# Optimization experiments

Measured on AMD Instinct MI355X. Metric: run time of the kernel, lower is better.

## Reference

```python
import jax, jax.numpy as jnp
import numpy as np

INPUT_SIZE = 512
HIDDEN_SIZE = 512
FORGET_BIAS = 1.0
B, T = 256, 256


def _xavier_uniform(key, shape):
    fan_out, fan_in = shape
    bound = jnp.sqrt(6.0 / (fan_in + fan_out))
    return jax.random.uniform(key, shape, jnp.float32, -bound, bound)


def setup_inputs() -> dict:
    key = jax.random.key(0)
    k1, k2, k3 = jax.random.split(key, 3)
    H, I = HIDDEN_SIZE, INPUT_SIZE
    x = jax.random.normal(k1, (B, T, I), jnp.float32)
    h0 = jnp.zeros((1, B, H), jnp.float32)
    c0 = jnp.zeros((1, B, H), jnp.float32)
    W_ih = _xavier_uniform(k2, (4 * H, I))
    W_hh = _xavier_uniform(k3, (4 * H, H))
    # biases init to zero, then forget_bias added to [H:2H] of BOTH biases (as in source)
    b = jnp.zeros((4 * H,), jnp.float32).at[H:2 * H].add(FORGET_BIAS)
    return {"input_tensor": x, "h0": h0, "c0": c0,
            "W_ih": W_ih, "W_hh": W_hh, "b_ih": b, "b_hh": b}


def reference(input_tensor, h0, c0, W_ih, W_hh, b_ih, b_hh):
    H = HIDDEN_SIZE
    half = H // 2
    b_all = b_ih + b_hh  # [4H]
    # precompute input projections for all timesteps: [T, B, 4H]
    x_proj = jnp.einsum('bti,gi->tbg', input_tensor, W_ih) + b_all

    def step(carry, xg):
        h, c, m = carry
        gates = xg + h @ W_hh.T                      # [B, 4H]
        i, f, g, o = jnp.split(gates, 4, axis=-1)
        c = jax.nn.sigmoid(f) * c + jax.nn.sigmoid(i) * jnp.tanh(g)
        h = jax.nn.sigmoid(o) * jnp.tanh(c)
        m = jnp.maximum(m, h[:, :half])              # running max over first half
        out = jnp.concatenate([m, h[:, half:]], axis=0)  # torch.cat default dim=0 -> [2B, half]
        return (h, c, m), out

    h_init = h0[0]
    c_init = c0[0]
    m_init = jnp.full((h_init.shape[0], half), -jnp.inf, h_init.dtype)
    (h_n, c_n, _), outs = jax.lax.scan(step, (h_init, c_init, m_init), x_proj)
    all_out = jnp.transpose(outs, (1, 0, 2))         # [2B, T, half]
    return all_out, h_n[None], c_n[None]
```

## Files before the change

### kernel.cpp

```cpp
#include <hip/hip_runtime.h>
#include <cstdint>

#define B_SZ 256
#define T_SZ 256
#define I_SZ 512
#define H_SZ 512
#define HALF 256

typedef __attribute__((ext_vector_type(8))) __bf16 bf16x8;
typedef __attribute__((ext_vector_type(8))) short short8;
typedef __attribute__((ext_vector_type(4))) float f32x4;
typedef __attribute__((ext_vector_type(4))) unsigned int uint4v;

__device__ __forceinline__ unsigned short f2bf(float f) {
  unsigned int u = __float_as_uint(f);
  u = (u + 0x7FFFu + ((u >> 16) & 1u)) >> 16;
  return (unsigned short)u;
}

__device__ __forceinline__ float sigm(float x) {
  return __builtin_amdgcn_rcpf(1.f + __expf(-x));
}
__device__ __forceinline__ float tanh_(float x) {
  float ax = fabsf(x);
  float e = __expf(-2.f * ax);
  float r = (1.f - e) * __builtin_amdgcn_rcpf(1.f + e);
  return copysignf(r, x);
}

__global__ void cvt_f32_bf16(const float* __restrict__ src, unsigned short* __restrict__ dst) {
  long i = ((long)blockIdx.x * 256 + threadIdx.x) * 8;
  float4 a = *(const float4*)(src + i);
  float4 b = *(const float4*)(src + i + 4);
  unsigned int w0 = (unsigned)f2bf(a.x) | ((unsigned)f2bf(a.y) << 16);
  unsigned int w1 = (unsigned)f2bf(a.z) | ((unsigned)f2bf(a.w) << 16);
  unsigned int w2 = (unsigned)f2bf(b.x) | ((unsigned)f2bf(b.y) << 16);
  unsigned int w3 = (unsigned)f2bf(b.z) | ((unsigned)f2bf(b.w) << 16);
  uint4v v = {w0, w1, w2, w3};
  *(uint4v*)(dst + i) = v;
}

__global__ void init_hw(const float* __restrict__ h0, unsigned long long* __restrict__ dst) {
  int i = blockIdx.x * 256 + threadIdx.x;
  unsigned int pw = (unsigned)f2bf(h0[2 * i]) | ((unsigned)f2bf(h0[2 * i + 1]) << 16);
  dst[65536 + i] = (unsigned long long)pw;
  dst[i] = 0xFFFFFFFF00000000ull;
}

__global__ void pack_w(const float* __restrict__ Wih, const float* __restrict__ Whh,
                       unsigned short* __restrict__ wp, unsigned short* __restrict__ hp) {
  int id = blockIdx.x * 256 + threadIdx.x;
  int cid = id & 131071;
  const float* W = (id < 131072) ? Wih : Whh;
  unsigned short* D = (id < 131072) ? wp : hp;
  int l  = cid & 63;
  int ks = (cid >> 6) & 15;
  int nt = (cid >> 10) & 1;
  int w  = (cid >> 11) & 3;
  int hg = (cid >> 13) & 15;
  int row = w * 512 + hg * 32 + nt * 16 + (l & 15);
  int k0  = ks * 32 + (l >> 4) * 8;
  const float* src = W + (long)row * 512 + k0;
  unsigned int wd[4];
#pragma unroll
  for (int j = 0; j < 4; ++j) {
    unsigned int lo = f2bf(src[2 * j]);
    unsigned int hi = f2bf(src[2 * j + 1]);
    wd[j] = lo | (hi << 16);
  }
  uint4v v = {wd[0], wd[1], wd[2], wd[3]};
  *(uint4v*)(D + (long)cid * 8) = v;
}

#define LDPA(dst, base, OFFSTR) \
  asm volatile("global_load_dwordx2 %0, %1, off offset:" OFFSTR " sc0" : "=v"(dst) : "v"(base))
#define LDPS(dst, base, OFFSTR) \
  asm volatile("global_load_dwordx2 %0, %1, off offset:" OFFSTR " sc0 sc1" : "=v"(dst) : "v"(base))
#define LDX16(dst, base, OFFSTR) \
  asm volatile("global_load_dwordx4 %0, %1, off offset:" OFFSTR : "=v"(dst) : "v"(base))

template <int SCOPE>
__device__ __forceinline__ void poll_check(unsigned long long* pv,
                                           const unsigned long long* srcb,
                                           int wv, unsigned tag) {
  bool redo = true;
  while (redo) {
    redo = false;
#pragma unroll
    for (int i = 0; i < 16; ++i) {
      if ((unsigned)(pv[i] >> 32) != tag) {
        const int row = 2 * wv + ((i >> 2) & 1) + (i >> 3) * 8;
        pv[i] = __hip_atomic_load(srcb + row * 256 + (i & 3), __ATOMIC_RELAXED, SCOPE);
        redo = true;
      }
    }
  }
}

template <int SCOPE>
__device__ __forceinline__ void st64(unsigned long long* p, unsigned long long v) {
  __hip_atomic_store(p, v, __ATOMIC_RELAXED, SCOPE);
}

__global__ __launch_bounds__(256, 1) void lstm_main(
    const unsigned short* __restrict__ xb,
    const float* __restrict__ c0,
    const float* __restrict__ b_ih, const float* __restrict__ b_hh,
    const unsigned short* __restrict__ wihp, const unsigned short* __restrict__ whhp,
    unsigned long long* __restrict__ hw64,
    unsigned long long* __restrict__ cnt64,
    float* __restrict__ out)
{
  const int tid  = threadIdx.x;
  const int lane = tid & 63;
  const int w    = tid >> 6;
  const int bg   = blockIdx.x & 15;
  const int hg   = blockIdx.x >> 4;
  const int s0   = hg * 32;
  const int q    = lane >> 4;
  const int c16  = lane & 15;

  __shared__ float glds[4 * 528];
  __shared__ __align__(16) unsigned int hpad[16 * 260];
  __shared__ int s_path;

  int xcd;
  asm volatile("s_getreg_b32 %0, hwreg(20, 0, 32)" : "=s"(xcd));
  xcd &= 15;
  if (tid == 0) {
    unsigned long long inc = 1ull << (8 * xcd);
    __hip_atomic_fetch_add(&cnt64[bg * 8], inc, __ATOMIC_RELAXED, __HIP_MEMORY_SCOPE_SYSTEM);
    unsigned long long m;
    do {
      __builtin_amdgcn_s_sleep(2);
      m = __hip_atomic_load(&cnt64[bg * 8], __ATOMIC_RELAXED, __HIP_MEMORY_SCOPE_SYSTEM);
    } while ((unsigned)((m * 0x0101010101010101ull) >> 56) < 16);
    s_path = (m == (16ull << (8 * xcd))) ? 1 : 0;
  }
  __syncthreads();
  const bool agent_path = (s_path != 0);

  bf16x8 wih[2][16], whh[2][16];
#pragma unroll
  for (int nt = 0; nt < 2; ++nt) {
#pragma unroll
    for (int ks = 0; ks < 16; ++ks) {
      int idc = ((hg * 4 + w) * 2 + nt) * 16 + ks;
      long off = ((long)(idc * 64 + lane)) * 8;
      wih[nt][ks] = __builtin_bit_cast(bf16x8, *(const short8*)(wihp + off));
      whh[nt][ks] = __builtin_bit_cast(bf16x8, *(const short8*)(whhp + off));
    }
  }

  const int jj  = tid & 31;
  const int bl0 = tid >> 5;
  const int bglob0 = bg * 16 + bl0;
  const int bglob1 = bglob0 + 8;
  float bias_v[4];
#pragma unroll
  for (int g = 0; g < 4; ++g)
    bias_v[g] = b_ih[g * 512 + s0 + jj] + b_hh[g * 512 + s0 + jj];
  float cst0 = c0[(long)bglob0 * H_SZ + s0 + jj];
  float cst1 = c0[(long)bglob1 * H_SZ + s0 + jj];
  float m0 = -INFINITY, m1 = -INFINITY;

  const unsigned short* xbase = xb + (long)(bg * 16 + c16) * T_SZ * I_SZ + q * 8;

  const int p   = tid >> 4;
  const int wv  = (tid >> 2) & 3;
  const int cq  = tid & 3;
  const int colbase = p * 16 + cq * 4;

  const int swz = (c16 & 7) << 2;

  bf16x8 xr[16];
  {
    const unsigned short* xn = xbase;
    LDX16(xr[0],  xn, "0");   LDX16(xr[1],  xn, "64");
    LDX16(xr[2],  xn, "128"); LDX16(xr[3],  xn, "192");
    LDX16(xr[4],  xn, "256"); LDX16(xr[5],  xn, "320");
    LDX16(xr[6],  xn, "384"); LDX16(xr[7],  xn, "448");
    LDX16(xr[8],  xn, "512"); LDX16(xr[9],  xn, "576");
    LDX16(xr[10], xn, "640"); LDX16(xr[11], xn, "704");
    LDX16(xr[12], xn, "768"); LDX16(xr[13], xn, "832");
    LDX16(xr[14], xn, "896"); LDX16(xr[15], xn, "960");
  }

#pragma unroll 1
  for (int t = 0; t < T_SZ; ++t) {
    asm volatile("s_waitcnt vmcnt(0)" ::: "memory");
    __builtin_amdgcn_sched_barrier(0);

    const unsigned long long* srcb = hw64 + ((t + 1) & 1) * 65536 + bg * 4096 + colbase;
    const unsigned long long* blo = srcb + 2 * wv * 256;
    const unsigned long long* bhi = blo + 8 * 256;
    unsigned long long pv[16];
    if (agent_path) {
      LDPA(pv[0],  blo, "0");    LDPA(pv[1],  blo, "8");
      LDPA(pv[2],  blo, "16");   LDPA(pv[3],  blo, "24");
      LDPA(pv[4],  blo, "2048"); LDPA(pv[5],  blo, "2056");
      LDPA(pv[6],  blo, "2064"); LDPA(pv[7],  blo, "2072");
      LDPA(pv[8],  bhi, "0");    LDPA(pv[9],  bhi, "8");
      LDPA(pv[10], bhi, "16");   LDPA(pv[11], bhi, "24");
      LDPA(pv[12], bhi, "2048"); LDPA(pv[13], bhi, "2056");
      LDPA(pv[14], bhi, "2064"); LDPA(pv[15], bhi, "2072");
    } else {
      LDPS(pv[0],  blo, "0");    LDPS(pv[1],  blo, "8");
      LDPS(pv[2],  blo, "16");   LDPS(pv[3],  blo, "24");
      LDPS(pv[4],  blo, "2048"); LDPS(pv[5],  blo, "2056");
      LDPS(pv[6],  blo, "2064"); LDPS(pv[7],  blo, "2072");
      LDPS(pv[8],  bhi, "0");    LDPS(pv[9],  bhi, "8");
      LDPS(pv[10], bhi, "16");   LDPS(pv[11], bhi, "24");
      LDPS(pv[12], bhi, "2048"); LDPS(pv[13], bhi, "2056");
      LDPS(pv[14], bhi, "2064"); LDPS(pv[15], bhi, "2072");
    }

    f32x4 acc0 = {0.f, 0.f, 0.f, 0.f};
    f32x4 acc1 = {0.f, 0.f, 0.f, 0.f};
#pragma unroll
    for (int ks = 0; ks < 16; ++ks) {
      bf16x8 a = xr[ks];
      acc0 = __builtin_amdgcn_mfma_f32_16x16x32_bf16(a, wih[0][ks], acc0, 0, 0, 0);
      acc1 = __builtin_amdgcn_mfma_f32_16x16x32_bf16(a, wih[1][ks], acc1, 0, 0, 0);
    }

    asm volatile("s_waitcnt vmcnt(0)" ::: "memory");
    __builtin_amdgcn_sched_barrier(0);

    if (agent_path) poll_check<__HIP_MEMORY_SCOPE_AGENT>(pv, srcb, wv, (unsigned)t);
    else            poll_check<__HIP_MEMORY_SCOPE_SYSTEM>(pv, srcb, wv, (unsigned)t);
#pragma unroll
    for (int g = 0; g < 4; ++g) {
      const int row = 2 * wv + (g & 1) + (g >> 1) * 8;
      const int pc  = colbase ^ ((row & 7) << 2);
      uint4v d = {(unsigned int)pv[g * 4 + 0], (unsigned int)pv[g * 4 + 1],
                  (unsigned int)pv[g * 4 + 2], (unsigned int)pv[g * 4 + 3]};
      *(uint4v*)(hpad + row * 260 + pc) = d;
    }
    __syncthreads();

    {
      const unsigned short* xn = xbase + (long)(t + 1 < T_SZ ? t + 1 : t) * I_SZ;
      LDX16(xr[0],  xn, "0");   LDX16(xr[1],  xn, "64");
      LDX16(xr[2],  xn, "128"); LDX16(xr[3],  xn, "192");
      LDX16(xr[4],  xn, "256"); LDX16(xr[5],  xn, "320");
      LDX16(xr[6],  xn, "384"); LDX16(xr[7],  xn, "448");
      LDX16(xr[8],  xn, "512"); LDX16(xr[9],  xn, "576");
      LDX16(xr[10], xn, "640"); LDX16(xr[11], xn, "704");
      LDX16(xr[12], xn, "768"); LDX16(xr[13], xn, "832");
      LDX16(xr[14], xn, "896"); LDX16(xr[15], xn, "960");
    }

    const unsigned int* hrow = hpad + c16 * 260;
#pragma unroll
    for (int ks = 0; ks < 16; ++ks) {
      bf16x8 a = __builtin_bit_cast(bf16x8,
                   *(const short8*)(hrow + ((ks * 16 + q * 4) ^ swz)));
      acc0 = __builtin_amdgcn_mfma_f32_16x16x32_bf16(a, whh[0][ks], acc0, 0, 0, 0);
      acc1 = __builtin_amdgcn_mfma_f32_16x16x32_bf16(a, whh[1][ks], acc1, 0, 0, 0);
    }

#pragma unroll
    for (int r = 0; r < 4; ++r) {
      glds[w * 528 + (q * 4 + r) * 33 + c16]      = acc0[r];
      glds[w * 528 + (q * 4 + r) * 33 + 16 + c16] = acc1[r];
    }
    __syncthreads();

    float hv0, hv1;
#pragma unroll
    for (int it = 0; it < 2; ++it) {
      int b = bl0 + it * 8;
      float gi = glds[0 * 528 + b * 33 + jj] + bias_v[0];
      float gf = glds[1 * 528 + b * 33 + jj] + bias_v[1];
      float gg = glds[2 * 528 + b * 33 + jj] + bias_v[2];
      float go = glds[3 * 528 + b * 33 + jj] + bias_v[3];
      float& cs = it ? cst1 : cst0;
      cs = sigm(gf) * cs + sigm(gi) * tanh_(gg);
      float h = sigm(go) * tanh_(cs);
      if (it) hv1 = h; else hv0 = h;
    }
    {
      float po0 = __shfl_xor(hv0, 1);
      float po1 = __shfl_xor(hv1, 1);
      if (!(jj & 1)) {
        unsigned long long tagw = (unsigned long long)(t + 1) << 32;
        unsigned long long w0 = tagw | ((unsigned)f2bf(hv0) | ((unsigned)f2bf(po0) << 16));
        unsigned long long w1 = tagw | ((unsigned)f2bf(hv1) | ((unsigned)f2bf(po1) << 16));
        unsigned long long* d0 = hw64 + (t & 1) * 65536 + bg * 4096
                               + bl0 * 256 + (s0 >> 1) + (jj >> 1);
        if (agent_path) {
          st64<__HIP_MEMORY_SCOPE_AGENT>(d0, w0);
          st64<__HIP_MEMORY_SCOPE_AGENT>(d0 + 8 * 256, w1);
        } else {
          st64<__HIP_MEMORY_SCOPE_SYSTEM>(d0, w0);
          st64<__HIP_MEMORY_SCOPE_SYSTEM>(d0 + 8 * 256, w1);
        }
      }
    }

#pragma unroll
    for (int it = 0; it < 2; ++it) {
      int b   = bl0 + it * 8;
      int bgl = bg * 16 + b;
      float h = it ? hv1 : hv0;
      float& mm = it ? m1 : m0;
      if (hg < 8) {
        mm = fmaxf(mm, h);
        out[(long)bgl * (T_SZ * HALF) + t * HALF + s0 + jj] = mm;
      } else {
        out[(long)(256 + bgl) * (T_SZ * HALF) + t * HALF + (s0 - 256) + jj] = h;
      }
      if (t == T_SZ - 1) {
        float cs = it ? cst1 : cst0;
        out[33554432L + (long)bgl * H_SZ + s0 + jj] = h;
        out[33554432L + 131072L + (long)bgl * H_SZ + s0 + jj] = cs;
      }
    }
  }
}

extern "C" void kernel_launch(void* const* d_in, const int* in_sizes, int n_in,
                              void* d_out, int out_size, void* d_ws, size_t ws_size,
                              hipStream_t stream) {
  const float* x   = (const float*)d_in[0];
  const float* h0  = (const float*)d_in[1];
  const float* c0  = (const float*)d_in[2];
  const float* Wih = (const float*)d_in[3];
  const float* Whh = (const float*)d_in[4];
  const float* bih = (const float*)d_in[5];
  const float* bhh = (const float*)d_in[6];
  float* out = (float*)d_out;

  char* ws = (char*)d_ws;
  unsigned short* xb     = (unsigned short*)(ws);
  unsigned short* wihp   = (unsigned short*)(ws + 67108864);
  unsigned short* whhp   = (unsigned short*)(ws + 69206016);
  unsigned long long* hw = (unsigned long long*)(ws + 71303168);
  unsigned long long* cn = (unsigned long long*)(ws + 72351744);

  hipMemsetAsync(cn, 0, 4096, stream);
  cvt_f32_bf16<<<16384, 256, 0, stream>>>(x, xb);
  init_hw<<<256, 256, 0, stream>>>(h0, hw);
  pack_w<<<1024, 256, 0, stream>>>(Wih, Whh, wihp, whhp);
  lstm_main<<<256, 256, 0, stream>>>(xb, c0, bih, bhh, wihp, whhp, hw, cn, out);
}
```

Before: 1.401 ms.

## Streamline per-step recurrence: fast poll check, split accumulators, lighter barriers

Restructures the per-timestep loop of the persistent LSTM kernel. The wait on the x prefetch is relaxed to vmcnt(3), and the tag check now runs a single fast test before falling back to the polling loop. Each MFMA chain is split into two independent accumulators to shorten dependency chains. __syncthreads is replaced by an explicit lgkmcnt wait plus s_barrier, the LDS XOR swizzle is removed, and the h-store work is split so odd and even lanes each issue one store. The risks are LDS bank conflicts from dropping the swizzle and a possibly wrong partial vmcnt wait.

```diff
diff --git a/kernel.cpp b/kernel.cpp
--- a/kernel.cpp
+++ b/kernel.cpp
@@ -80,9 +80,9 @@
   asm volatile("global_load_dwordx4 %0, %1, off offset:" OFFSTR : "=v"(dst) : "v"(base))
 
 template <int SCOPE>
-__device__ __forceinline__ void poll_check(unsigned long long* pv,
-                                           const unsigned long long* srcb,
-                                           int wv, unsigned tag) {
+__device__ __forceinline__ void poll_slow(unsigned long long* pv,
+                                          const unsigned long long* srcb,
+                                          int wv, unsigned tag) {
   bool redo = true;
   while (redo) {
     redo = false;
@@ -171,8 +171,6 @@
   const int cq  = tid & 3;
   const int colbase = p * 16 + cq * 4;
 
-  const int swz = (c16 & 7) << 2;
-
   bf16x8 xr[16];
   {
     const unsigned short* xn = xbase;
@@ -185,10 +183,12 @@
     LDX16(xr[12], xn, "768"); LDX16(xr[13], xn, "832");
     LDX16(xr[14], xn, "896"); LDX16(xr[15], xn, "960");
   }
+  asm volatile("s_waitcnt vmcnt(0)" ::: "memory");
+  __builtin_amdgcn_sched_barrier(0);
 
 #pragma unroll 1
   for (int t = 0; t < T_SZ; ++t) {
-    asm volatile("s_waitcnt vmcnt(0)" ::: "memory");
+    asm volatile("s_waitcnt vmcnt(3)" ::: "memory");
     __builtin_amdgcn_sched_barrier(0);
 
     const unsigned long long* srcb = hw64 + ((t + 1) & 1) * 65536 + bg * 4096 + colbase;
@@ -215,29 +215,42 @@
       LDPS(pv[14], bhi, "2064"); LDPS(pv[15], bhi, "2072");
     }
 
-    f32x4 acc0 = {0.f, 0.f, 0.f, 0.f};
-    f32x4 acc1 = {0.f, 0.f, 0.f, 0.f};
-#pragma unroll
-    for (int ks = 0; ks < 16; ++ks) {
-      bf16x8 a = xr[ks];
-      acc0 = __builtin_amdgcn_mfma_f32_16x16x32_bf16(a, wih[0][ks], acc0, 0, 0, 0);
-      acc1 = __builtin_amdgcn_mfma_f32_16x16x32_bf16(a, wih[1][ks], acc1, 0, 0, 0);
+    f32x4 a0a = {0.f, 0.f, 0.f, 0.f};
+    f32x4 a0b = {0.f, 0.f, 0.f, 0.f};
+    f32x4 a1a = {0.f, 0.f, 0.f, 0.f};
+    f32x4 a1b = {0.f, 0.f, 0.f, 0.f};
+#pragma unroll
+    for (int ks = 0; ks < 16; ks += 2) {
+      a0a = __builtin_amdgcn_mfma_f32_16x16x32_bf16(xr[ks],     wih[0][ks],     a0a, 0, 0, 0);
+      a1a = __builtin_amdgcn_mfma_f32_16x16x32_bf16(xr[ks],     wih[1][ks],     a1a, 0, 0, 0);
+      a0b = __builtin_amdgcn_mfma_f32_16x16x32_bf16(xr[ks + 1], wih[0][ks + 1], a0b, 0, 0, 0);
+      a1b = __builtin_amdgcn_mfma_f32_16x16x32_bf16(xr[ks + 1], wih[1][ks + 1], a1b, 0, 0, 0);
     }
 
     asm volatile("s_waitcnt vmcnt(0)" ::: "memory");
     __builtin_amdgcn_sched_barrier(0);
 
-    if (agent_path) poll_check<__HIP_MEMORY_SCOPE_AGENT>(pv, srcb, wv, (unsigned)t);
-    else            poll_check<__HIP_MEMORY_SCOPE_SYSTEM>(pv, srcb, wv, (unsigned)t);
+    {
+      unsigned ok = 1u;
+#pragma unroll
+      for (int i = 0; i < 16; ++i) ok &= ((unsigned)(pv[i] >> 32) == (unsigned)t) ? 1u : 0u;
+      if (__builtin_expect(ok == 0u, 0)) {
+        if (agent_path) poll_slow<__HIP_MEMORY_SCOPE_AGENT>(pv, srcb, wv, (unsigned)t);
+        else            poll_slow<__HIP_MEMORY_SCOPE_SYSTEM>(pv, srcb, wv, (unsigned)t);
+      }
+    }
+
 #pragma unroll
     for (int g = 0; g < 4; ++g) {
       const int row = 2 * wv + (g & 1) + (g >> 1) * 8;
-      const int pc  = colbase ^ ((row & 7) << 2);
       uint4v d = {(unsigned int)pv[g * 4 + 0], (unsigned int)pv[g * 4 + 1],
                   (unsigned int)pv[g * 4 + 2], (unsigned int)pv[g * 4 + 3]};
-      *(uint4v*)(hpad + row * 260 + pc) = d;
-    }
-    __syncthreads();
+      *(uint4v*)(hpad + row * 260 + colbase) = d;
+    }
+    asm volatile("s_waitcnt lgkmcnt(0)" ::: "memory");
+    __builtin_amdgcn_s_barrier();
+    asm volatile("" ::: "memory");
+    __builtin_amdgcn_sched_barrier(0);
 
     {
       const unsigned short* xn = xbase + (long)(t + 1 < T_SZ ? t + 1 : t) * I_SZ;
@@ -253,19 +266,26 @@
 
     const unsigned int* hrow = hpad + c16 * 260;
 #pragma unroll
-    for (int ks = 0; ks < 16; ++ks) {
-      bf16x8 a = __builtin_bit_cast(bf16x8,
-                   *(const short8*)(hrow + ((ks * 16 + q * 4) ^ swz)));
-      acc0 = __builtin_amdgcn_mfma_f32_16x16x32_bf16(a, whh[0][ks], acc0, 0, 0, 0);
-      acc1 = __builtin_amdgcn_mfma_f32_16x16x32_bf16(a, whh[1][ks], acc1, 0, 0, 0);
-    }
+    for (int ks = 0; ks < 16; ks += 2) {
+      bf16x8 aa = __builtin_bit_cast(bf16x8, *(const short8*)(hrow + ks * 16 + q * 4));
+      bf16x8 ab = __builtin_bit_cast(bf16x8, *(const short8*)(hrow + (ks + 1) * 16 + q * 4));
+      a0a = __builtin_amdgcn_mfma_f32_16x16x32_bf16(aa, whh[0][ks],     a0a, 0, 0, 0);
+      a1a = __builtin_amdgcn_mfma_f32_16x16x32_bf16(aa, whh[1][ks],     a1a, 0, 0, 0);
+      a0b = __builtin_amdgcn_mfma_f32_16x16x32_bf16(ab, whh[0][ks + 1], a0b, 0, 0, 0);
+      a1b = __builtin_amdgcn_mfma_f32_16x16x32_bf16(ab, whh[1][ks + 1], a1b, 0, 0, 0);
+    }
+    f32x4 acc0 = a0a + a0b;
+    f32x4 acc1 = a1a + a1b;
 
 #pragma unroll
     for (int r = 0; r < 4; ++r) {
       glds[w * 528 + (q * 4 + r) * 33 + c16]      = acc0[r];
       glds[w * 528 + (q * 4 + r) * 33 + 16 + c16] = acc1[r];
     }
-    __syncthreads();
+    asm volatile("s_waitcnt lgkmcnt(0)" ::: "memory");
+    __builtin_amdgcn_s_barrier();
+    asm volatile("" ::: "memory");
+    __builtin_amdgcn_sched_barrier(0);
 
     float hv0, hv1;
 #pragma unroll
@@ -283,20 +303,20 @@
     {
       float po0 = __shfl_xor(hv0, 1);
       float po1 = __shfl_xor(hv1, 1);
+      unsigned long long tagw = (unsigned long long)(t + 1) << 32;
+      unsigned long long* d0 = hw64 + (t & 1) * 65536 + bg * 4096
+                             + bl0 * 256 + (s0 >> 1) + (jj >> 1);
+      unsigned long long wrd;
+      unsigned long long* dst;
       if (!(jj & 1)) {
-        unsigned long long tagw = (unsigned long long)(t + 1) << 32;
-        unsigned long long w0 = tagw | ((unsigned)f2bf(hv0) | ((unsigned)f2bf(po0) << 16));
-        unsigned long long w1 = tagw | ((unsigned)f2bf(hv1) | ((unsigned)f2bf(po1) << 16));
-        unsigned long long* d0 = hw64 + (t & 1) * 65536 + bg * 4096
-                               + bl0 * 256 + (s0 >> 1) + (jj >> 1);
-        if (agent_path) {
-          st64<__HIP_MEMORY_SCOPE_AGENT>(d0, w0);
-          st64<__HIP_MEMORY_SCOPE_AGENT>(d0 + 8 * 256, w1);
-        } else {
-          st64<__HIP_MEMORY_SCOPE_SYSTEM>(d0, w0);
-          st64<__HIP_MEMORY_SCOPE_SYSTEM>(d0 + 8 * 256, w1);
-        }
-      }
+        wrd = tagw | ((unsigned)f2bf(hv0) | ((unsigned)f2bf(po0) << 16));
+        dst = d0;
+      } else {
+        wrd = tagw | ((unsigned)f2bf(po1) | ((unsigned)f2bf(hv1) << 16));
+        dst = d0 + 8 * 256;
+      }
+      if (agent_path) st64<__HIP_MEMORY_SCOPE_AGENT>(dst, wrd);
+      else            st64<__HIP_MEMORY_SCOPE_SYSTEM>(dst, wrd);
     }
 
 #pragma unroll
```

Measured after the change: 1.651 ms. 1.18x slower.

## Assign block roles dynamically by XCD to co-locate batch groups

Applied to the files above, without the earlier changes.

Each block now takes a slot from a global per-XCD arrival counter after a grid-wide rendezvous and derives its batch group and hidden group from that slot. The goal is to place the 16 blocks of one batch group on the same XCD so they can use agent-scope polling rather than system-scope. The XOR swizzle on the LDS hidden-state buffer is also removed, since the 260-word row padding already staggers banks. This adds a global barrier at startup and depends on how blocks are actually distributed across XCDs.

```diff
diff --git a/kernel.cpp b/kernel.cpp
--- a/kernel.cpp
+++ b/kernel.cpp
@@ -114,31 +114,52 @@
   const int tid  = threadIdx.x;
   const int lane = tid & 63;
   const int w    = tid >> 6;
-  const int bg   = blockIdx.x & 15;
-  const int hg   = blockIdx.x >> 4;
-  const int s0   = hg * 32;
   const int q    = lane >> 4;
   const int c16  = lane & 15;
 
   __shared__ float glds[4 * 528];
   __shared__ __align__(16) unsigned int hpad[16 * 260];
-  __shared__ int s_path;
+  __shared__ int s_bg, s_hg, s_agent;
 
   int xcd;
   asm volatile("s_getreg_b32 %0, hwreg(20, 0, 32)" : "=s"(xcd));
-  xcd &= 15;
+  xcd &= 7;
   if (tid == 0) {
-    unsigned long long inc = 1ull << (8 * xcd);
-    __hip_atomic_fetch_add(&cnt64[bg * 8], inc, __ATOMIC_RELAXED, __HIP_MEMORY_SCOPE_SYSTEM);
-    unsigned long long m;
+    unsigned long long old = __hip_atomic_fetch_add(
+        &cnt64[0], 1ull << (8 * xcd), __ATOMIC_RELAXED, __HIP_MEMORY_SCOPE_SYSTEM);
+    int r = (int)((old >> (8 * xcd)) & 0xFF);
+    __hip_atomic_fetch_add(&cnt64[1], 1ull, __ATOMIC_RELEASE, __HIP_MEMORY_SCOPE_SYSTEM);
+    unsigned long long tot;
     do {
       __builtin_amdgcn_s_sleep(2);
-      m = __hip_atomic_load(&cnt64[bg * 8], __ATOMIC_RELAXED, __HIP_MEMORY_SCOPE_SYSTEM);
-    } while ((unsigned)((m * 0x0101010101010101ull) >> 56) < 16);
-    s_path = (m == (16ull << (8 * xcd))) ? 1 : 0;
+      tot = __hip_atomic_load(&cnt64[1], __ATOMIC_ACQUIRE, __HIP_MEMORY_SCOPE_SYSTEM);
+    } while (tot < 256);
+    unsigned long long cnts =
+        __hip_atomic_load(&cnt64[0], __ATOMIC_RELAXED, __HIP_MEMORY_SCOPE_SYSTEM);
+    int base = 0;
+#pragma unroll
+    for (int x2 = 0; x2 < 8; ++x2) {
+      int c = (int)((cnts >> (8 * x2)) & 0xFF);
+      if (x2 < xcd) base += c;
+    }
+    int slot = base + r;
+    s_bg = slot >> 4;
+    s_hg = slot & 15;
+    int g0 = slot & ~15;
+    int acc = 0, ag = 0;
+#pragma unroll
+    for (int x2 = 0; x2 < 8; ++x2) {
+      int c = (int)((cnts >> (8 * x2)) & 0xFF);
+      if (g0 >= acc && g0 + 16 <= acc + c) ag = 1;
+      acc += c;
+    }
+    s_agent = ag;
   }
   __syncthreads();
-  const bool agent_path = (s_path != 0);
+  const int bg = s_bg;
+  const int hg = s_hg;
+  const bool agent_path = (s_agent != 0);
+  const int s0 = hg * 32;
 
   bf16x8 wih[2][16], whh[2][16];
 #pragma unroll
@@ -170,8 +191,6 @@
   const int wv  = (tid >> 2) & 3;
   const int cq  = tid & 3;
   const int colbase = p * 16 + cq * 4;
-
-  const int swz = (c16 & 7) << 2;
 
   bf16x8 xr[16];
   {
@@ -232,10 +251,9 @@
 #pragma unroll
     for (int g = 0; g < 4; ++g) {
       const int row = 2 * wv + (g & 1) + (g >> 1) * 8;
-      const int pc  = colbase ^ ((row & 7) << 2);
       uint4v d = {(unsigned int)pv[g * 4 + 0], (unsigned int)pv[g * 4 + 1],
                   (unsigned int)pv[g * 4 + 2], (unsigned int)pv[g * 4 + 3]};
-      *(uint4v*)(hpad + row * 260 + pc) = d;
+      *(uint4v*)(hpad + row * 260 + colbase) = d;
     }
     __syncthreads();
 
@@ -254,8 +272,7 @@
     const unsigned int* hrow = hpad + c16 * 260;
 #pragma unroll
     for (int ks = 0; ks < 16; ++ks) {
-      bf16x8 a = __builtin_bit_cast(bf16x8,
-                   *(const short8*)(hrow + ((ks * 16 + q * 4) ^ swz)));
+      bf16x8 a = __builtin_bit_cast(bf16x8, *(const short8*)(hrow + ks * 16 + q * 4));
       acc0 = __builtin_amdgcn_mfma_f32_16x16x32_bf16(a, whh[0][ks], acc0, 0, 0, 0);
       acc1 = __builtin_amdgcn_mfma_f32_16x16x32_bf16(a, whh[1][ks], acc1, 0, 0, 0);
     }
```

Result: no change. 1.399 ms (-0.1%).
